# Kernel optimization log

Hardware: AMD Instinct MI355X
Metric: run time of the kernel (lower is better)

Reference implementation:

```python
import jax, jax.numpy as jnp
import numpy as np

B, C, H, W = 2, 256, 64, 64
HEADS = 8
HEAD_DIM = C // HEADS  # 32
INNER = HEADS * HEAD_DIM  # 256
GROUPS = 32
EPS = 1e-5


def groupnorm(x, w, b):
    # x: [B, C, H, W]; normalize over (C//G, H, W) within each of G groups
    Bx, Cx, Hx, Wx = x.shape
    xg = x.reshape(Bx, GROUPS, -1)
    mu = xg.mean(axis=-1, keepdims=True)
    var = xg.var(axis=-1, keepdims=True)
    xn = ((xg - mu) * jax.lax.rsqrt(var + EPS)).reshape(Bx, Cx, Hx, Wx)
    return xn * w[:, None, None] + b[:, None, None]


def setup_inputs() -> dict:
    key = jax.random.key(0)
    k0, k1, k2 = jax.random.split(key, 3)
    x = jax.random.normal(k0, (B, C, H, W), dtype=jnp.float32)
    gn_weight = jnp.ones((C,), dtype=jnp.float32)
    gn_bias = jnp.zeros((C,), dtype=jnp.float32)
    # 1x1 conv weights (kernel dims squeezed): [out_ch, in_ch]
    w_qkv = jax.random.normal(k1, (3 * INNER, C), dtype=jnp.float32) * 0.02
    w_out = jax.random.normal(k2, (C, INNER), dtype=jnp.float32) * 0.02
    return {"x": x, "gn_weight": gn_weight, "gn_bias": gn_bias,
            "w_qkv": w_qkv, "w_out": w_out}


def reference(x, gn_weight, gn_bias, w_qkv, w_out):
    Bx, Cx, Hx, Wx = x.shape
    N = Hx * Wx
    scale = HEAD_DIM ** -0.5
    xn = groupnorm(x, gn_weight, gn_bias)
    # 1x1 conv == channel matmul
    qkv = jnp.einsum('oc,bchw->bohw', w_qkv, xn)  # [B, 3*INNER, H, W]
    q, k, v = jnp.split(qkv, 3, axis=1)
    # 'b (h d) x y -> b h (x y) d'
    def to_heads(t):
        return t.reshape(Bx, HEADS, HEAD_DIM, N).transpose(0, 1, 3, 2)  # bhnd
    q, k, v = to_heads(q), to_heads(k), to_heads(v)
    sim = jnp.einsum('bhid,bhjd->bhij', q, k) * scale  # [B, h, N, N]
    attn = jax.nn.softmax(sim, axis=-1)
    o = jnp.einsum('bhij,bhjd->bhid', attn, v)  # [B, h, N, d]
    # 'b h (x y) d -> b (h d) x y'
    o = o.transpose(0, 1, 3, 2).reshape(Bx, INNER, Hx, Wx)
    out = jnp.einsum('co,bohw->bchw', w_out, o)
    return x + out
```

## Files before the change

kernel.cpp:

```cpp
#include <hip/hip_runtime.h>
#include <hip/hip_bf16.h>

#define BATCH 2
#define CH 256
#define HW 4096
#define HEADS 8
#define HDIM 32
#define GROUPS 32
#define EPS 1e-5f
#define SCALE 0.17677669529663687f
#define QSCALE (0.17677669529663687f * 1.4426950408889634f)

typedef short s16x8 __attribute__((ext_vector_type(8)));
typedef float floatx4 __attribute__((ext_vector_type(4)));
typedef unsigned short ushort_t;
typedef unsigned int uint_t;

static __device__ __forceinline__ ushort_t f2bf(float f) {
    __hip_bfloat16 h = __float2bfloat16(f);
    return *reinterpret_cast<ushort_t*>(&h);
}

static __device__ __forceinline__ uint_t pk2(float lo, float hi) {
    return __builtin_amdgcn_perm(__float_as_uint(hi), __float_as_uint(lo), 0x07060302u);
}

static __device__ __forceinline__ void gload_lds16(const ushort_t* g, ushort_t* l) {
    __builtin_amdgcn_global_load_lds((const __attribute__((address_space(1))) void*)g,
                                     (__attribute__((address_space(3))) void*)l, 16, 0, 0);
}

__global__ void gn_stats_wcvt(const float* __restrict__ x, float* __restrict__ stats,
                              const float* __restrict__ wq, const float* __restrict__ wo,
                              ushort_t* __restrict__ wdst) {
    if (blockIdx.x >= 64) {
        int i = (blockIdx.x - 64) * 256 + threadIdx.x;
        float4 v = (i < 49152) ? ((const float4*)wq)[i] : ((const float4*)wo)[i - 49152];
        ushort_t p[4] = {f2bf(v.x), f2bf(v.y), f2bf(v.z), f2bf(v.w)};
        uint2 o;
        o.x = (uint_t)p[0] | ((uint_t)p[1] << 16);
        o.y = (uint_t)p[2] | ((uint_t)p[3] << 16);
        *(uint2*)&wdst[(size_t)i * 4] = o;
        return;
    }
    int bg = blockIdx.x;
    const float4* xv = (const float4*)(x + (size_t)bg * 8 * HW);
    int t = threadIdx.x;
    float s = 0.f, ss = 0.f;
    for (int i = t; i < 8192; i += 256) {
        float4 v = xv[i];
        s  += v.x + v.y + v.z + v.w;
        ss += v.x*v.x + v.y*v.y + v.z*v.z + v.w*v.w;
    }
    #pragma unroll
    for (int off = 32; off; off >>= 1) {
        s  += __shfl_down(s, off);
        ss += __shfl_down(ss, off);
    }
    __shared__ float rs[4], rss[4];
    int wave = t >> 6;
    if ((t & 63) == 0) { rs[wave] = s; rss[wave] = ss; }
    __syncthreads();
    if (t == 0) {
        s  = rs[0] + rs[1] + rs[2] + rs[3];
        ss = rss[0] + rss[1] + rss[2] + rss[3];
        float mu  = s / 32768.f;
        float var = ss / 32768.f - mu * mu;
        stats[bg * 2]     = mu;
        stats[bg * 2 + 1] = rsqrtf(var + EPS);
    }
}

__global__ void norm_transpose(const float* __restrict__ x, const float* __restrict__ stats,
                               const float* __restrict__ gw, const float* __restrict__ gb,
                               ushort_t* __restrict__ xn) {
    __shared__ ushort_t tile[64][40];
    int b = blockIdx.z, c0 = blockIdx.y * 32, n0 = blockIdx.x * 64;
    int t = threadIdx.x;
    #pragma unroll
    for (int i = 0; i < 8; i++) {
        int idx = i * 256 + t;
        int c = idx >> 6, n = idx & 63;
        int cc = c0 + c;
        float mu   = stats[(b * GROUPS + (cc >> 3)) * 2];
        float rstd = stats[(b * GROUPS + (cc >> 3)) * 2 + 1];
        float v = x[((size_t)b * CH + cc) * HW + n0 + n];
        v = (v - mu) * rstd * gw[cc] + gb[cc];
        tile[n][c] = f2bf(v);
    }
    __syncthreads();
    int n = t >> 2, chk = t & 3;
    uint4 val = *(const uint4*)&tile[n][chk * 8];
    *(uint4*)(xn + ((size_t)(b * HW + n0 + n)) * CH + c0 + chk * 8) = val;
}

__global__ void qkv_gemm(const ushort_t* __restrict__ xn, const ushort_t* __restrict__ wqb,
                         ushort_t* __restrict__ qo, ushort_t* __restrict__ ko,
                         ushort_t* __restrict__ vo) {
    __shared__ ushort_t Al[64][40];
    __shared__ ushort_t Bl[64][40];
    int b = blockIdx.z;
    int n0 = blockIdx.x * 64, o0 = blockIdx.y * 64;
    int t = threadIdx.x, lane = t & 63, wave = t >> 6;
    int lr = lane & 15, lk = lane >> 4;
    int row = t >> 2, chk = t & 3;
    const ushort_t* asrc = xn + ((size_t)(b * HW + n0 + row)) * CH + chk * 8;
    const ushort_t* bsrc = wqb + (size_t)(o0 + row) * CH + chk * 8;
    floatx4 acc[4] = {};
    uint4 ra = *(const uint4*)(asrc);
    uint4 rb = *(const uint4*)(bsrc);
    for (int k0 = 0; k0 < 8; k0++) {
        *(uint4*)&Al[row][chk * 8] = ra;
        *(uint4*)&Bl[row][chk * 8] = rb;
        __syncthreads();
        if (k0 < 7) {
            ra = *(const uint4*)(asrc + (k0 + 1) * 32);
            rb = *(const uint4*)(bsrc + (k0 + 1) * 32);
        }
        s16x8 af = *(const s16x8*)&Al[wave * 16 + lr][lk * 8];
        #pragma unroll
        for (int ct = 0; ct < 4; ct++) {
            s16x8 bf = *(const s16x8*)&Bl[ct * 16 + lr][lk * 8];
            acc[ct] = __builtin_amdgcn_mfma_f32_16x16x32_bf16(af, bf, acc[ct], 0, 0, 0);
        }
        __syncthreads();
    }
    #pragma unroll
    for (int ct = 0; ct < 4; ct++) {
        int o = o0 + ct * 16 + lr;
        int sel = o >> 8;
        int h = (o >> 5) & 7;
        int d = o & 31;
        int nrow0 = n0 + wave * 16 + (lk << 2);
        if (sel == 0) {
            #pragma unroll
            for (int r = 0; r < 4; r++)
                qo[(((size_t)(b * HEADS + h)) * HW + nrow0 + r) * HDIM + d] =
                    f2bf(acc[ct][r] * QSCALE);
        } else if (sel == 1) {
            #pragma unroll
            for (int r = 0; r < 4; r++) {
                int tt = (nrow0 + r) & 63;
                int sg = 4 * ((tt >> 3) & 3) + 16 * ((((tt >> 2) & 1) << 1) | ((tt >> 5) & 1)) + (tt & 3);
                ko[(((size_t)(b * HEADS + h)) * HW + n0 + sg) * HDIM + d] = f2bf(acc[ct][r]);
            }
        } else {
            ushort_t pk[4];
            #pragma unroll
            for (int r = 0; r < 4; r++) pk[r] = f2bf(acc[ct][r]);
            *(uint2*)&vo[(((size_t)(b * HEADS + h)) * HDIM + d) * HW + nrow0] = *(uint2*)pk;
        }
    }
}

__global__ void __launch_bounds__(256, 2)
attn9(const ushort_t* __restrict__ qg, const ushort_t* __restrict__ kg,
      const ushort_t* __restrict__ vg, ushort_t* __restrict__ og) {
    __shared__ ushort_t Kl[2][2048];
    __shared__ ushort_t Vl[2][2048];
    const int bh = blockIdx.y;
    const int n0 = blockIdx.x * 128;
    const int t = threadIdx.x;
    const int lane = t & 63, w = t >> 6;
    const int lr = lane & 15, lk = lane >> 4;

    const ushort_t* kb = kg + (size_t)bh * HW * HDIM;
    const ushort_t* vb = vg + (size_t)bh * HDIM * HW;

    const int lrr = t & 15, lkk = (t >> 4) & 3, wv = t >> 6;
    const ushort_t* gk = kb + ((wv << 4) + lrr) * HDIM + lkk * 8;
    const ushort_t* gv = vb + (size_t)(((t >> 7) << 4) + lrr) * HW + ((t >> 6) & 1) * 32 + lkk * 8;
    ushort_t* kd0 = &Kl[0][wv << 9]; ushort_t* kd1 = &Kl[1][wv << 9];
    ushort_t* vd0 = &Vl[0][wv << 9]; ushort_t* vd1 = &Vl[1][wv << 9];

    s16x8 qf0 = *(const s16x8*)(qg + ((size_t)bh * HW + n0 + w * 16 + lr) * HDIM + lk * 8);
    s16x8 qf1 = *(const s16x8*)(qg + ((size_t)bh * HW + n0 + 64 + w * 16 + lr) * HDIM + lk * 8);
    asm volatile("s_waitcnt vmcnt(0)" ::: "memory");

    const s16x8 onesf = {0x3F80, 0x3F80, 0x3F80, 0x3F80, 0x3F80, 0x3F80, 0x3F80, 0x3F80};
    const floatx4 zf = {};
    floatx4 oacc[2][2] = {};
    floatx4 Lacc[2] = {};

    auto stage = [&](ushort_t* kdn, ushort_t* vdn) {
        gload_lds16(gk, kdn);
        gload_lds16(gv, vdn);
        gk += 64 * HDIM; gv += 64;
    };
    auto compute = [&](const ushort_t* Kb, const ushort_t* Vb) {
        floatx4 sim0[4], sim1[4];
        __builtin_amdgcn_s_setprio(1);
#pragma unroll
        for (int ct = 0; ct < 4; ct++) {
            s16x8 kf = *(const s16x8*)(Kb + ct * 512 + lane * 8);
            sim0[ct] = __builtin_amdgcn_mfma_f32_16x16x32_bf16(kf, qf0, zf, 0, 0, 0);
            sim1[ct] = __builtin_amdgcn_mfma_f32_16x16x32_bf16(kf, qf1, zf, 0, 0, 0);
        }
        __builtin_amdgcn_s_setprio(0);
        s16x8 vf[4];
#pragma unroll
        for (int i = 0; i < 4; i++)
            vf[i] = *(const s16x8*)(Vb + i * 512 + lane * 8);
        {
            s16x8 pf[2];
#pragma unroll
            for (int s = 0; s < 2; s++) {
                union { uint_t u[4]; s16x8 v; } pu;
                pu.u[0] = pk2(__builtin_amdgcn_exp2f(sim0[s][0]),     __builtin_amdgcn_exp2f(sim0[s][1]));
                pu.u[1] = pk2(__builtin_amdgcn_exp2f(sim0[s][2]),     __builtin_amdgcn_exp2f(sim0[s][3]));
                pu.u[2] = pk2(__builtin_amdgcn_exp2f(sim0[s + 2][0]), __builtin_amdgcn_exp2f(sim0[s + 2][1]));
                pu.u[3] = pk2(__builtin_amdgcn_exp2f(sim0[s + 2][2]), __builtin_amdgcn_exp2f(sim0[s + 2][3]));
                pf[s] = pu.v;
            }
            __builtin_amdgcn_s_setprio(1);
#pragma unroll
            for (int s = 0; s < 2; s++) {
                oacc[0][0] = __builtin_amdgcn_mfma_f32_16x16x32_bf16(vf[s],     pf[s], oacc[0][0], 0, 0, 0);
                oacc[0][1] = __builtin_amdgcn_mfma_f32_16x16x32_bf16(vf[2 + s], pf[s], oacc[0][1], 0, 0, 0);
                Lacc[0]    = __builtin_amdgcn_mfma_f32_16x16x32_bf16(onesf,     pf[s], Lacc[0],    0, 0, 0);
            }
            __builtin_amdgcn_s_setprio(0);
        }
        {
            s16x8 pf[2];
#pragma unroll
            for (int s = 0; s < 2; s++) {
                union { uint_t u[4]; s16x8 v; } pu;
                pu.u[0] = pk2(__builtin_amdgcn_exp2f(sim1[s][0]),     __builtin_amdgcn_exp2f(sim1[s][1]));
                pu.u[1] = pk2(__builtin_amdgcn_exp2f(sim1[s][2]),     __builtin_amdgcn_exp2f(sim1[s][3]));
                pu.u[2] = pk2(__builtin_amdgcn_exp2f(sim1[s + 2][0]), __builtin_amdgcn_exp2f(sim1[s + 2][1]));
                pu.u[3] = pk2(__builtin_amdgcn_exp2f(sim1[s + 2][2]), __builtin_amdgcn_exp2f(sim1[s + 2][3]));
                pf[s] = pu.v;
            }
            __builtin_amdgcn_s_setprio(1);
#pragma unroll
            for (int s = 0; s < 2; s++) {
                oacc[1][0] = __builtin_amdgcn_mfma_f32_16x16x32_bf16(vf[s],     pf[s], oacc[1][0], 0, 0, 0);
                oacc[1][1] = __builtin_amdgcn_mfma_f32_16x16x32_bf16(vf[2 + s], pf[s], oacc[1][1], 0, 0, 0);
                Lacc[1]    = __builtin_amdgcn_mfma_f32_16x16x32_bf16(onesf,     pf[s], Lacc[1],    0, 0, 0);
            }
            __builtin_amdgcn_s_setprio(0);
        }
    };

#define SYNCF { asm volatile("s_waitcnt vmcnt(0)" ::: "memory"); __syncthreads(); }

    stage(kd0, vd0);
    SYNCF
    for (int s2 = 0; s2 < 32; s2++) {
        stage(kd1, vd1);
        compute(&Kl[0][0], &Vl[0][0]);
        SYNCF
        if (s2 < 31) {
            stage(kd0, vd0);
            compute(&Kl[1][0], &Vl[1][0]);
            SYNCF
        } else {
            compute(&Kl[1][0], &Vl[1][0]);
        }
    }
#undef SYNCF

    const int b = bh >> 3, h = bh & 7;
#pragma unroll
    for (int c = 0; c < 2; c++) {
        float inv = 1.0f / Lacc[c][0];
        int n = n0 + c * 64 + w * 16 + lr;
#pragma unroll
        for (int ct2 = 0; ct2 < 2; ct2++) {
            uint_t lo = (uint_t)f2bf(oacc[c][ct2][0] * inv) | ((uint_t)f2bf(oacc[c][ct2][1] * inv) << 16);
            uint_t hi = (uint_t)f2bf(oacc[c][ct2][2] * inv) | ((uint_t)f2bf(oacc[c][ct2][3] * inv) << 16);
            uint2 val = {lo, hi};
            *(uint2*)(og + ((size_t)b * HW + n) * CH + h * 32 + ct2 * 16 + lk * 4) = val;
        }
    }
}

__global__ void proj_res(const ushort_t* __restrict__ oa, const ushort_t* __restrict__ wob,
                         const float* __restrict__ x, float* __restrict__ out) {
    __shared__ ushort_t Al[64][40];
    __shared__ ushort_t Bl[64][40];
    int m0 = blockIdx.x * 64;
    int c0 = blockIdx.y * 64;
    int t = threadIdx.x, lane = t & 63, wave = t >> 6;
    int lr = lane & 15, lk = lane >> 4;
    int row = t >> 2, chk = t & 3;
    const ushort_t* asrc = oa + (size_t)(m0 + row) * CH + chk * 8;
    const ushort_t* bsrc = wob + (size_t)(c0 + row) * CH + chk * 8;
    floatx4 acc[4] = {};
    uint4 ra = *(const uint4*)(asrc);
    uint4 rb = *(const uint4*)(bsrc);
    for (int k0 = 0; k0 < 8; k0++) {
        *(uint4*)&Al[row][chk * 8] = ra;
        *(uint4*)&Bl[row][chk * 8] = rb;
        __syncthreads();
        if (k0 < 7) {
            ra = *(const uint4*)(asrc + (k0 + 1) * 32);
            rb = *(const uint4*)(bsrc + (k0 + 1) * 32);
        }
        s16x8 af = *(const s16x8*)&Al[wave * 16 + lr][lk * 8];
        #pragma unroll
        for (int ct = 0; ct < 4; ct++) {
            s16x8 bf = *(const s16x8*)&Bl[ct * 16 + lr][lk * 8];
            acc[ct] = __builtin_amdgcn_mfma_f32_16x16x32_bf16(af, bf, acc[ct], 0, 0, 0);
        }
        __syncthreads();
    }
    int mrow0 = m0 + wave * 16 + (lk << 2);
    int b = mrow0 >> 12;
    int n = mrow0 & 4095;
    #pragma unroll
    for (int ct = 0; ct < 4; ct++) {
        int c = c0 + ct * 16 + lr;
        const float4 xv = *(const float4*)(x + ((size_t)(b * CH + c)) * HW + n);
        float4 ov;
        ov.x = acc[ct][0] + xv.x;
        ov.y = acc[ct][1] + xv.y;
        ov.z = acc[ct][2] + xv.z;
        ov.w = acc[ct][3] + xv.w;
        *(float4*)(out + ((size_t)(b * CH + c)) * HW + n) = ov;
    }
}

extern "C" void kernel_launch(void* const* d_in, const int* in_sizes, int n_in,
                              void* d_out, int out_size, void* d_ws, size_t ws_size,
                              hipStream_t stream) {
    const float* x    = (const float*)d_in[0];
    const float* gw   = (const float*)d_in[1];
    const float* gb   = (const float*)d_in[2];
    const float* wqkv = (const float*)d_in[3];
    const float* wout = (const float*)d_in[4];
    float* out = (float*)d_out;

    char* ws = (char*)d_ws;
    float* stats = (float*)ws;
    ushort_t* xn = (ushort_t*)(ws + 512);
    size_t per = (size_t)BATCH * HW * CH;
    ushort_t* q   = xn + per;
    ushort_t* k   = q + per;
    ushort_t* v   = k + per;
    ushort_t* oa  = v + per;
    ushort_t* wqb = oa + per;
    ushort_t* wob = wqb + 196608;

    gn_stats_wcvt<<<320, 256, 0, stream>>>(x, stats, wqkv, wout, wqb);
    norm_transpose<<<dim3(64, 8, 2), 256, 0, stream>>>(x, stats, gw, gb, xn);
    qkv_gemm<<<dim3(64, 12, 2), 256, 0, stream>>>(xn, wqb, q, k, v);
    attn9<<<dim3(32, 16), 256, 0, stream>>>(q, k, v, oa);
    proj_res<<<dim3(128, 4), 256, 0, stream>>>(oa, wob, x, out);
}
```

Before: 88.88 us.

## Split attention over two KV halves and merge partial outputs in separate kernel

```diff
diff --git a/kernel.cpp b/kernel.cpp
--- a/kernel.cpp
+++ b/kernel.cpp
@@ -19,6 +19,9 @@
 static __device__ __forceinline__ ushort_t f2bf(float f) {
     __hip_bfloat16 h = __float2bfloat16(f);
     return *reinterpret_cast<ushort_t*>(&h);
+}
+static __device__ __forceinline__ float bf2f(uint_t u) {
+    return __uint_as_float(u << 16);
 }
 
 static __device__ __forceinline__ uint_t pk2(float lo, float hi) {
@@ -153,19 +156,21 @@
     }
 }
 
-__global__ void __launch_bounds__(256, 2)
-attn9(const ushort_t* __restrict__ qg, const ushort_t* __restrict__ kg,
-      const ushort_t* __restrict__ vg, ushort_t* __restrict__ og) {
+__global__ void __launch_bounds__(256, 4)
+attn10(const ushort_t* __restrict__ qg, const ushort_t* __restrict__ kg,
+       const ushort_t* __restrict__ vg, ushort_t* __restrict__ op0,
+       ushort_t* __restrict__ op1, float* __restrict__ lpart) {
     __shared__ ushort_t Kl[2][2048];
     __shared__ ushort_t Vl[2][2048];
     const int bh = blockIdx.y;
+    const int z = blockIdx.z;
     const int n0 = blockIdx.x * 128;
     const int t = threadIdx.x;
     const int lane = t & 63, w = t >> 6;
     const int lr = lane & 15, lk = lane >> 4;
 
-    const ushort_t* kb = kg + (size_t)bh * HW * HDIM;
-    const ushort_t* vb = vg + (size_t)bh * HDIM * HW;
+    const ushort_t* kb = kg + (size_t)bh * HW * HDIM + (size_t)z * 2048 * HDIM;
+    const ushort_t* vb = vg + (size_t)bh * HDIM * HW + z * 2048;
 
     const int lrr = t & 15, lkk = (t >> 4) & 3, wv = t >> 6;
     const ushort_t* gk = kb + ((wv << 4) + lrr) * HDIM + lkk * 8;
@@ -247,11 +252,11 @@
 
     stage(kd0, vd0);
     SYNCF
-    for (int s2 = 0; s2 < 32; s2++) {
+    for (int s2 = 0; s2 < 16; s2++) {
         stage(kd1, vd1);
         compute(&Kl[0][0], &Vl[0][0]);
         SYNCF
-        if (s2 < 31) {
+        if (s2 < 15) {
             stage(kd0, vd0);
             compute(&Kl[1][0], &Vl[1][0]);
             SYNCF
@@ -261,19 +266,44 @@
     }
 #undef SYNCF
 
-    const int b = bh >> 3, h = bh & 7;
+    ushort_t* ob = (z ? op1 : op0) + ((size_t)bh * HW) * 32;
+    float* lp = lpart + (size_t)(z * 16 + bh) * HW;
 #pragma unroll
     for (int c = 0; c < 2; c++) {
-        float inv = 1.0f / Lacc[c][0];
         int n = n0 + c * 64 + w * 16 + lr;
+        if (lk == 0) lp[n] = Lacc[c][0];
 #pragma unroll
         for (int ct2 = 0; ct2 < 2; ct2++) {
-            uint_t lo = (uint_t)f2bf(oacc[c][ct2][0] * inv) | ((uint_t)f2bf(oacc[c][ct2][1] * inv) << 16);
-            uint_t hi = (uint_t)f2bf(oacc[c][ct2][2] * inv) | ((uint_t)f2bf(oacc[c][ct2][3] * inv) << 16);
+            uint_t lo = (uint_t)f2bf(oacc[c][ct2][0]) | ((uint_t)f2bf(oacc[c][ct2][1]) << 16);
+            uint_t hi = (uint_t)f2bf(oacc[c][ct2][2]) | ((uint_t)f2bf(oacc[c][ct2][3]) << 16);
             uint2 val = {lo, hi};
-            *(uint2*)(og + ((size_t)b * HW + n) * CH + h * 32 + ct2 * 16 + lk * 4) = val;
-        }
-    }
+            *(uint2*)(ob + (size_t)n * 32 + ct2 * 16 + lk * 4) = val;
+        }
+    }
+}
+
+__global__ void attn_merge(const ushort_t* __restrict__ op0, const ushort_t* __restrict__ op1,
+                           const float* __restrict__ lpart, ushort_t* __restrict__ oa) {
+    int idx = blockIdx.x * 256 + threadIdx.x;
+    int chunk = idx & 3;
+    int n = (idx >> 2) & 4095;
+    int bh = idx >> 14;
+    size_t base = ((size_t)bh * HW + n) * 32 + chunk * 8;
+    uint4 a = *(const uint4*)(op0 + base);
+    uint4 bq = *(const uint4*)(op1 + base);
+    float L = lpart[(size_t)bh * HW + n] + lpart[(size_t)(16 + bh) * HW + n];
+    float inv = 1.0f / L;
+    uint_t ua[4] = {a.x, a.y, a.z, a.w}, ub[4] = {bq.x, bq.y, bq.z, bq.w};
+    ushort_t res[8];
+#pragma unroll
+    for (int i = 0; i < 4; i++) {
+        float lo = bf2f(ua[i] & 0xffffu) + bf2f(ub[i] & 0xffffu);
+        float hi = bf2f(ua[i] >> 16) + bf2f(ub[i] >> 16);
+        res[2 * i]     = f2bf(lo * inv);
+        res[2 * i + 1] = f2bf(hi * inv);
+    }
+    ushort_t* dst = oa + ((size_t)((bh >> 3) * HW) + n) * CH + (bh & 7) * 32 + chunk * 8;
+    *(uint4*)dst = *(uint4*)res;
 }
 
 __global__ void proj_res(const ushort_t* __restrict__ oa, const ushort_t* __restrict__ wob,
@@ -342,10 +372,14 @@
     ushort_t* oa  = v + per;
     ushort_t* wqb = oa + per;
     ushort_t* wob = wqb + 196608;
+    ushort_t* op1 = wob + 65536;
+    float* lpart  = (float*)(op1 + per);
+    ushort_t* op0 = xn;
 
     gn_stats_wcvt<<<320, 256, 0, stream>>>(x, stats, wqkv, wout, wqb);
     norm_transpose<<<dim3(64, 8, 2), 256, 0, stream>>>(x, stats, gw, gb, xn);
     qkv_gemm<<<dim3(64, 12, 2), 256, 0, stream>>>(xn, wqb, q, k, v);
-    attn9<<<dim3(32, 16), 256, 0, stream>>>(q, k, v, oa);
+    attn10<<<dim3(32, 16, 2), 256, 0, stream>>>(q, k, v, op0, op1, lpart);
+    attn_merge<<<1024, 256, 0, stream>>>(op0, op1, lpart, oa);
     proj_res<<<dim3(128, 4), 256, 0, stream>>>(oa, wob, x, out);
 }
```

Result: faster. 84.42 us (-5.0%).
